# Kernel tuning notes

Measured on AMD Instinct MI355X. Metric: run time of the kernel, lower is better.

Reference implementation:

```python
import jax, jax.numpy as jnp
import numpy as np

B, T, C, H = 2, 2048, 1024, 16
D = C // H  # head dim 64

def setup_inputs() -> dict:
    key = jax.random.key(0)
    k1, k2, k3 = jax.random.split(key, 3)
    x = jax.random.normal(k1, (B, T, C), dtype=jnp.float32)
    W_attn = jax.random.normal(k2, (C, 3 * C), dtype=jnp.float32) * (1.0 / np.sqrt(C))
    b_attn = jnp.zeros((3 * C,), dtype=jnp.float32)
    W_proj = jax.random.normal(k3, (C, C), dtype=jnp.float32) * (1.0 / np.sqrt(C))
    b_proj = jnp.zeros((C,), dtype=jnp.float32)
    return {"x": x, "W_attn": W_attn, "b_attn": b_attn, "W_proj": W_proj, "b_proj": b_proj}

def reference(x, W_attn, b_attn, W_proj, b_proj):
    Bsz, Tlen, Cdim = x.shape
    qkv = x @ W_attn + b_attn  # [B,T,3C]
    q, k, v = jnp.split(qkv, 3, axis=2)
    # [B,T,C] -> [B,H,T,D]
    q = q.reshape(Bsz, Tlen, H, D).transpose(0, 2, 1, 3)
    k = k.reshape(Bsz, Tlen, H, D).transpose(0, 2, 1, 3)
    v = v.reshape(Bsz, Tlen, H, D).transpose(0, 2, 1, 3)
    att = jnp.einsum('bhqd,bhkd->bhqk', q, k) * (1.0 / np.sqrt(D))
    causal = jnp.tril(jnp.ones((Tlen, Tlen), dtype=bool))
    att = jnp.where(causal[None, None, :, :], att, jnp.float32(-jnp.inf))
    att = jax.nn.softmax(att, axis=-1)
    y = jnp.einsum('bhqk,bhkd->bhqd', att, v)  # [B,H,T,D]
    y = y.transpose(0, 2, 1, 3).reshape(Bsz, Tlen, Cdim)
    return y @ W_proj + b_proj
```

## Files before the change

### kernel.cpp

```cpp
#include <hip/hip_runtime.h>
#include <math.h>

#define BSZ 2
#define TSEQ 2048
#define CDIM 1024
#define HNUM 16

typedef __attribute__((ext_vector_type(8))) short bhalf8;
typedef __attribute__((ext_vector_type(4))) short bhalf4;
typedef __attribute__((ext_vector_type(4))) float floatx4;

__device__ __forceinline__ unsigned short f2bf(float f) {
    union { float f; unsigned u; } v;
    v.f = f;
    unsigned r = v.u + 0x7FFFu + ((v.u >> 16) & 1u);
    return (unsigned short)(r >> 16);
}

__device__ __forceinline__ floatx4 fx4_zero() { floatx4 z = {0.f,0.f,0.f,0.f}; return z; }

typedef __attribute__((address_space(3))) unsigned int lds_u32;
typedef const __attribute__((address_space(1))) unsigned int g_u32;
__device__ __forceinline__ void async_copy16(const void* g, void* l) {
    __builtin_amdgcn_global_load_lds((g_u32*)g, (lds_u32*)l, 16, 0, 0);
}

__global__ __launch_bounds__(256) void conv_bf16(
    const float* __restrict__ x, unsigned short* __restrict__ xb)
{
    size_t i = ((size_t)blockIdx.x * 256 + threadIdx.x) * 8;
    float4 a = *(const float4*)(x + i);
    float4 b = *(const float4*)(x + i + 4);
    uint4 o;
    o.x = (unsigned)f2bf(a.x) | ((unsigned)f2bf(a.y) << 16);
    o.y = (unsigned)f2bf(a.z) | ((unsigned)f2bf(a.w) << 16);
    o.z = (unsigned)f2bf(b.x) | ((unsigned)f2bf(b.y) << 16);
    o.w = (unsigned)f2bf(b.z) | ((unsigned)f2bf(b.w) << 16);
    *(uint4*)(xb + i) = o;
}

__global__ __launch_bounds__(256) void transpose_bf16(
    const float* __restrict__ W, unsigned short* __restrict__ Wt, int K, int N)
{
    __shared__ float t[32][33];
    const int n0 = blockIdx.x * 32, k0 = blockIdx.y * 32;
    const int tx = threadIdx.x & 31, ty = threadIdx.x >> 5;
#pragma unroll
    for (int i = 0; i < 4; ++i)
        t[ty + i * 8][tx] = W[(size_t)(k0 + ty + i * 8) * N + n0 + tx];
    __syncthreads();
#pragma unroll
    for (int i = 0; i < 4; ++i)
        Wt[(size_t)(n0 + ty + i * 8) * K + k0 + tx] = f2bf(t[tx][ty + i * 8]);
}

template<int BM, bool OUT_BF16>
__global__ __launch_bounds__(256) void gemm_bt(
    const unsigned short* __restrict__ A, const unsigned short* __restrict__ Bt,
    const float* __restrict__ bias, void* __restrict__ Cp,
    int M, int N, int K, int v_start, unsigned short* __restrict__ vt)
{
    constexpr int ALINES = BM / 64;
    constexpr int MT = BM / 32;
    __shared__ unsigned short As[2][BM * 32];
    __shared__ unsigned short Bs[2][128 * 32];

    const int tid   = threadIdx.x;
    const int bm    = blockIdx.y;
    const int bn    = blockIdx.x;
    const int wave  = tid >> 6;
    const int col16 = tid & 15;
    const int quad  = (tid & 63) >> 4;
    const int wm    = (wave >> 1) * (BM / 2);
    const int wn    = (wave & 1) * 64;

    floatx4 acc[MT][4];
#pragma unroll
    for (int i = 0; i < MT; ++i)
#pragma unroll
        for (int j = 0; j < 4; ++j) acc[i][j] = fx4_zero();

    const int gr = tid >> 2;
    const int gk = (tid & 3) * 8;
    const unsigned short* Ab = A  + (size_t)(bm * BM + gr) * K + gk;
    const unsigned short* Bb = Bt + (size_t)(bn * 128 + gr) * K + gk;

#define STAGE(k0, bf) { \
    char* AsB = (char*)As[bf] + wave * 1024; \
    char* BsB = (char*)Bs[bf] + wave * 1024; \
    _Pragma("unroll") \
    for (int l = 0; l < ALINES; ++l) \
        async_copy16(Ab + (size_t)l * 64 * K + (k0), AsB + l * 4096); \
    async_copy16(Bb + (k0), BsB); \
    async_copy16(Bb + (size_t)64 * K + (k0), BsB + 4096); }

#define COMPUTE(bf) { \
    bhalf8 a[MT], b[4]; \
    _Pragma("unroll") \
    for (int i = 0; i < MT; ++i) \
        a[i] = *(const bhalf8*)&As[bf][(wm + i * 16 + col16) * 32 + quad * 8]; \
    _Pragma("unroll") \
    for (int j = 0; j < 4; ++j) \
        b[j] = *(const bhalf8*)&Bs[bf][(wn + j * 16 + col16) * 32 + quad * 8]; \
    _Pragma("unroll") \
    for (int i = 0; i < MT; ++i) \
        _Pragma("unroll") \
        for (int j = 0; j < 4; ++j) \
            acc[i][j] = __builtin_amdgcn_mfma_f32_16x16x32_bf16(a[i], b[j], acc[i][j], 0, 0, 0); }

    STAGE(0, 0);
    __syncthreads();
    int buf = 0;
    for (int k0 = 0; k0 < K - 32; k0 += 32) {
        STAGE(k0 + 32, buf ^ 1);
        COMPUTE(buf);
        __syncthreads();
        buf ^= 1;
    }
    COMPUTE(buf);
#undef STAGE
#undef COMPUTE

    const int colbase = bn * 128 + wn;
    const bool vpath = (v_start >= 0) && (colbase >= v_start);
#pragma unroll
    for (int j = 0; j < 4; ++j) {
        int col = colbase + j * 16 + col16;
        float bv = bias[col];
#pragma unroll
        for (int i = 0; i < MT; ++i) {
            if (vpath) {
                int row0 = bm * BM + wm + i * 16 + quad * 4;
                ushort4 o;
                o.x = f2bf(acc[i][j][0] + bv);
                o.y = f2bf(acc[i][j][1] + bv);
                o.z = f2bf(acc[i][j][2] + bv);
                o.w = f2bf(acc[i][j][3] + bv);
                size_t vrow = (size_t)((row0 >> 11) * 1024 + (col - v_start));
                *(ushort4*)(vt + vrow * 2048 + (row0 & 2047)) = o;
            } else {
#pragma unroll
                for (int r = 0; r < 4; ++r) {
                    int row = bm * BM + wm + i * 16 + quad * 4 + r;
                    float v = acc[i][j][r] + bv;
                    if (OUT_BF16)
                        ((unsigned short*)Cp)[(size_t)row * N + col] = f2bf(v);
                    else
                        ((float*)Cp)[(size_t)row * N + col] = v;
                }
            }
        }
    }
}

template<bool DIAG>
__device__ __forceinline__ void attn_tile(
    const unsigned short* __restrict__ Ks, const unsigned short* __restrict__ Vt,
    const bhalf8* qf, floatx4* oT, float& l_part,
    int col16, int quad, int qloc)
{
    const float C_MUL = 0.125f * 1.44269504f;
    const float C_SUB = 17.31234049f;
    const int sx = col16 & 7;

    floatx4 s[4];
#pragma unroll
    for (int n = 0; n < 4; ++n) {
        const int row = 16 * n + col16;
        bhalf8 k0 = *(const bhalf8*)&Ks[row * 64 + ((quad ^ sx) * 8)];
        bhalf8 k1 = *(const bhalf8*)&Ks[row * 64 + (((4 + quad) ^ sx) * 8)];
        floatx4 t = __builtin_amdgcn_mfma_f32_16x16x32_bf16(k0, qf[0], fx4_zero(), 0, 0, 0);
        s[n] = __builtin_amdgcn_mfma_f32_16x16x32_bf16(k1, qf[1], t, 0, 0, 0);
    }

    bhalf4 pb[4];
#pragma unroll
    for (int n = 0; n < 4; ++n) {
        unsigned a[4];
#pragma unroll
        for (int r = 0; r < 4; ++r) {
            float p = exp2f(fmaf(s[n][r], C_MUL, -C_SUB));
            if (DIAG) {
                if (16 * n + quad * 4 + r > qloc) p = 0.f;
            }
            l_part += p;
            a[r] = __float_as_uint(p) + 0x8000u;
        }
        union { unsigned u[2]; bhalf4 b; } uu;
        uu.u[0] = (a[0] >> 16) | (a[1] & 0xffff0000u);
        uu.u[1] = (a[2] >> 16) | (a[3] & 0xffff0000u);
        pb[n] = uu.b;
    }

#pragma unroll
    for (int n = 0; n < 4; ++n) {
#pragma unroll
        for (int dt = 0; dt < 4; ++dt) {
            const int d = 16 * dt + col16;
            const bhalf4 av = *(const bhalf4*)&Vt[d * 76 + 16 * n + quad * 4];
            oT[dt] = __builtin_amdgcn_mfma_f32_16x16x16bf16_1k(av, pb[n], oT[dt], 0, 0, 0);
        }
    }
}

__global__ __launch_bounds__(256) void attn_mfma(
    const unsigned short* __restrict__ qkv,
    const unsigned short* __restrict__ vT,
    unsigned short* __restrict__ yout)
{
    __shared__ unsigned short Kbuf[2][64 * 64];
    __shared__ unsigned short Vbuf[2][64 * 76];

    const int tid   = threadIdx.x;
    const int wave  = tid >> 6;
    const int col16 = tid & 15;
    const int quad  = (tid & 63) >> 4;
    const int qb    = (int)gridDim.y - 1 - (int)blockIdx.y;
    const int bh    = blockIdx.x;
    const int b     = bh >> 4;
    const int h     = bh & 15;

    const unsigned short* base  = qkv + (size_t)b * TSEQ * 3072 + h * 64;
    const unsigned short* kbase = base + CDIM;
    const unsigned short* vtb   = vT + (size_t)(b * 1024 + h * 64) * 2048;

    bhalf8 qf[2];
    {
        const unsigned short* qrow =
            base + (size_t)(qb * 64 + wave * 16 + col16) * 3072 + quad * 8;
        qf[0] = *(const bhalf8*)qrow;
        qf[1] = *(const bhalf8*)(qrow + 32);
    }

    const int krow = tid >> 3;
    const int kchk = (tid & 7) ^ (krow & 7);
    const unsigned short* ksrc0 = kbase + (size_t)krow * 3072 + kchk * 8;
    const unsigned short* ksrc1 = kbase + (size_t)(krow + 32) * 3072 + kchk * 8;

    const int vd  = tid >> 3;
    const int vt0 = (tid & 7) * 8;
    const unsigned short* vsrc0 = vtb + (size_t)vd * 2048 + vt0;
    const unsigned short* vsrc1 = vtb + (size_t)(vd + 32) * 2048 + vt0;

#define KSTAGE(kb, bf) { \
    char* Kd = (char*)Kbuf[bf] + wave * 1024; \
    async_copy16(ksrc0 + (size_t)(kb) * 64 * 3072, Kd); \
    async_copy16(ksrc1 + (size_t)(kb) * 64 * 3072, Kd + 4096); }

    floatx4 oT[4];
#pragma unroll
    for (int dt = 0; dt < 4; ++dt) oT[dt] = fx4_zero();
    float l_part = 0.f;
    const int qloc = wave * 16 + col16;

    {
        uint4 nv0 = *(const uint4*)vsrc0;
        uint4 nv1 = *(const uint4*)vsrc1;
        KSTAGE(0, 0);
        *(uint4*)&Vbuf[0][vd * 76 + vt0]        = nv0;
        *(uint4*)&Vbuf[0][(vd + 32) * 76 + vt0] = nv1;
    }
    __syncthreads();
    int buf = 0;
    for (int kb = 0; kb < qb; ++kb) {
        uint4 nv0 = *(const uint4*)(vsrc0 + (size_t)(kb + 1) * 64);
        uint4 nv1 = *(const uint4*)(vsrc1 + (size_t)(kb + 1) * 64);
        KSTAGE(kb + 1, buf ^ 1);
        attn_tile<false>(Kbuf[buf], Vbuf[buf], qf, oT, l_part, col16, quad, qloc);
        *(uint4*)&Vbuf[buf ^ 1][vd * 76 + vt0]        = nv0;
        *(uint4*)&Vbuf[buf ^ 1][(vd + 32) * 76 + vt0] = nv1;
        __syncthreads();
        buf ^= 1;
    }
    attn_tile<true>(Kbuf[buf], Vbuf[buf], qf, oT, l_part, col16, quad, qloc);
#undef KSTAGE

    float l = l_part;
    l += __shfl_xor(l, 16);
    l += __shfl_xor(l, 32);
    const float inv = 1.0f / l;
    const size_t row = (size_t)b * TSEQ + (size_t)qb * 64 + wave * 16 + col16;
#pragma unroll
    for (int dt = 0; dt < 4; ++dt) {
        ushort4 o;
        o.x = f2bf(oT[dt][0] * inv);
        o.y = f2bf(oT[dt][1] * inv);
        o.z = f2bf(oT[dt][2] * inv);
        o.w = f2bf(oT[dt][3] * inv);
        *(ushort4*)(yout + row * CDIM + h * 64 + 16 * dt + quad * 4) = o;
    }
}

extern "C" void kernel_launch(void* const* d_in, const int* in_sizes, int n_in,
                              void* d_out, int out_size, void* d_ws, size_t ws_size,
                              hipStream_t stream)
{
    const float* x      = (const float*)d_in[0];
    const float* W_attn = (const float*)d_in[1];
    const float* b_attn = (const float*)d_in[2];
    const float* W_proj = (const float*)d_in[3];
    const float* b_proj = (const float*)d_in[4];
    float* out = (float*)d_out;

    unsigned short* qkv = (unsigned short*)d_ws;
    unsigned short* y   = qkv + (size_t)4096 * 3072;
    unsigned short* xb  = y   + (size_t)4096 * 1024;
    unsigned short* WtA = xb  + (size_t)4096 * 1024;
    unsigned short* WtP = WtA + (size_t)3072 * 1024;
    unsigned short* vT  = WtP + (size_t)1024 * 1024;

    conv_bf16<<<dim3((4096 * 1024) / (256 * 8)), 256, 0, stream>>>(x, xb);
    transpose_bf16<<<dim3(3072 / 32, 1024 / 32), 256, 0, stream>>>(W_attn, WtA, 1024, 3072);
    transpose_bf16<<<dim3(1024 / 32, 1024 / 32), 256, 0, stream>>>(W_proj, WtP, 1024, 1024);

    gemm_bt<128, true><<<dim3(3072 / 128, 4096 / 128), 256, 0, stream>>>(
        xb, WtA, b_attn, qkv, 4096, 3072, 1024, 2048, vT);
    attn_mfma<<<dim3(BSZ * HNUM, TSEQ / 64), 256, 0, stream>>>(qkv, vT, y);
    gemm_bt<64, false><<<dim3(1024 / 128, 4096 / 64), 256, 0, stream>>>(
        y, WtP, b_proj, out, 4096, 1024, 1024, -1, nullptr);
}
```

Before: 188.4 us.

## Fuse prepass kernels, split-K projection, and widen attention blocks to 128 queries

Merges the input conversion and two weight transposes into one prepass launch. Splits the output projection GEMM over two K halves that accumulate into a zeroed output with atomic adds. Moves attention to 512-thread blocks covering 128 query rows, where each K/V tile is loaded once per block and shared by more waves, and the softmax exponent prep uses packed float2 math. The changes target launch overhead, reuse of K/V loads, and projection parallelism, at the cost of an extra memset, atomic traffic on the output, and fewer attention blocks with more threads each.

```diff
diff --git a/kernel.cpp b/kernel.cpp
--- a/kernel.cpp
+++ b/kernel.cpp
@@ -9,6 +9,7 @@
 typedef __attribute__((ext_vector_type(8))) short bhalf8;
 typedef __attribute__((ext_vector_type(4))) short bhalf4;
 typedef __attribute__((ext_vector_type(4))) float floatx4;
+typedef __attribute__((ext_vector_type(2))) float floatx2;
 
 __device__ __forceinline__ unsigned short f2bf(float f) {
     union { float f; unsigned u; } v;
@@ -25,26 +26,11 @@
     __builtin_amdgcn_global_load_lds((g_u32*)g, (lds_u32*)l, 16, 0, 0);
 }
 
-__global__ __launch_bounds__(256) void conv_bf16(
-    const float* __restrict__ x, unsigned short* __restrict__ xb)
-{
-    size_t i = ((size_t)blockIdx.x * 256 + threadIdx.x) * 8;
-    float4 a = *(const float4*)(x + i);
-    float4 b = *(const float4*)(x + i + 4);
-    uint4 o;
-    o.x = (unsigned)f2bf(a.x) | ((unsigned)f2bf(a.y) << 16);
-    o.y = (unsigned)f2bf(a.z) | ((unsigned)f2bf(a.w) << 16);
-    o.z = (unsigned)f2bf(b.x) | ((unsigned)f2bf(b.y) << 16);
-    o.w = (unsigned)f2bf(b.z) | ((unsigned)f2bf(b.w) << 16);
-    *(uint4*)(xb + i) = o;
-}
-
-__global__ __launch_bounds__(256) void transpose_bf16(
-    const float* __restrict__ W, unsigned short* __restrict__ Wt, int K, int N)
-{
-    __shared__ float t[32][33];
-    const int n0 = blockIdx.x * 32, k0 = blockIdx.y * 32;
-    const int tx = threadIdx.x & 31, ty = threadIdx.x >> 5;
+__device__ __forceinline__ void trans_tile(
+    const float* __restrict__ W, unsigned short* __restrict__ Wt,
+    int K, int N, int n0, int k0, int tid, float (*t)[33])
+{
+    const int tx = tid & 31, ty = tid >> 5;
 #pragma unroll
     for (int i = 0; i < 4; ++i)
         t[ty + i * 8][tx] = W[(size_t)(k0 + ty + i * 8) * N + n0 + tx];
@@ -54,15 +40,39 @@
         Wt[(size_t)(n0 + ty + i * 8) * K + k0 + tx] = f2bf(t[tx][ty + i * 8]);
 }
 
-template<int BM, bool OUT_BF16>
-__global__ __launch_bounds__(256) void gemm_bt(
+__global__ __launch_bounds__(256) void prepass(
+    const float* __restrict__ x, unsigned short* __restrict__ xb,
+    const float* __restrict__ Wa, unsigned short* __restrict__ WtA,
+    const float* __restrict__ Wp, unsigned short* __restrict__ WtP)
+{
+    __shared__ float t[32][33];
+    const int bid = blockIdx.x;
+    const int tid = threadIdx.x;
+    if (bid < 2048) {
+        size_t i = ((size_t)bid * 256 + tid) * 8;
+        float4 a = *(const float4*)(x + i);
+        float4 b = *(const float4*)(x + i + 4);
+        uint4 o;
+        o.x = (unsigned)f2bf(a.x) | ((unsigned)f2bf(a.y) << 16);
+        o.y = (unsigned)f2bf(a.z) | ((unsigned)f2bf(a.w) << 16);
+        o.z = (unsigned)f2bf(b.x) | ((unsigned)f2bf(b.y) << 16);
+        o.w = (unsigned)f2bf(b.z) | ((unsigned)f2bf(b.w) << 16);
+        *(uint4*)(xb + i) = o;
+    } else if (bid < 5120) {
+        int tl = bid - 2048;
+        trans_tile(Wa, WtA, 1024, 3072, (tl % 96) * 32, (tl / 96) * 32, tid, t);
+    } else {
+        int tl = bid - 5120;
+        trans_tile(Wp, WtP, 1024, 1024, (tl % 32) * 32, (tl / 32) * 32, tid, t);
+    }
+}
+
+__global__ __launch_bounds__(256) void gemm_qkv(
     const unsigned short* __restrict__ A, const unsigned short* __restrict__ Bt,
-    const float* __restrict__ bias, void* __restrict__ Cp,
+    const float* __restrict__ bias, unsigned short* __restrict__ Cp,
     int M, int N, int K, int v_start, unsigned short* __restrict__ vt)
 {
-    constexpr int ALINES = BM / 64;
-    constexpr int MT = BM / 32;
-    __shared__ unsigned short As[2][BM * 32];
+    __shared__ unsigned short As[2][128 * 32];
     __shared__ unsigned short Bs[2][128 * 32];
 
     const int tid   = threadIdx.x;
@@ -71,66 +81,65 @@
     const int wave  = tid >> 6;
     const int col16 = tid & 15;
     const int quad  = (tid & 63) >> 4;
-    const int wm    = (wave >> 1) * (BM / 2);
+    const int wm    = (wave >> 1) * 64;
     const int wn    = (wave & 1) * 64;
 
-    floatx4 acc[MT][4];
-#pragma unroll
-    for (int i = 0; i < MT; ++i)
+    floatx4 acc[4][4];
+#pragma unroll
+    for (int i = 0; i < 4; ++i)
 #pragma unroll
         for (int j = 0; j < 4; ++j) acc[i][j] = fx4_zero();
 
     const int gr = tid >> 2;
     const int gk = (tid & 3) * 8;
-    const unsigned short* Ab = A  + (size_t)(bm * BM + gr) * K + gk;
+    const unsigned short* Ab = A  + (size_t)(bm * 128 + gr) * K + gk;
     const unsigned short* Bb = Bt + (size_t)(bn * 128 + gr) * K + gk;
 
-#define STAGE(k0, bf) { \
+#define QSTAGE(k0, bf) { \
     char* AsB = (char*)As[bf] + wave * 1024; \
     char* BsB = (char*)Bs[bf] + wave * 1024; \
-    _Pragma("unroll") \
-    for (int l = 0; l < ALINES; ++l) \
-        async_copy16(Ab + (size_t)l * 64 * K + (k0), AsB + l * 4096); \
-    async_copy16(Bb + (k0), BsB); \
+    async_copy16(Ab + (k0),                  AsB); \
+    async_copy16(Ab + (size_t)64 * K + (k0), AsB + 4096); \
+    async_copy16(Bb + (k0),                  BsB); \
     async_copy16(Bb + (size_t)64 * K + (k0), BsB + 4096); }
 
-#define COMPUTE(bf) { \
-    bhalf8 a[MT], b[4]; \
-    _Pragma("unroll") \
-    for (int i = 0; i < MT; ++i) \
+#define QCOMPUTE(bf) { \
+    bhalf8 a[4], b[4]; \
+    _Pragma("unroll") \
+    for (int i = 0; i < 4; ++i) \
         a[i] = *(const bhalf8*)&As[bf][(wm + i * 16 + col16) * 32 + quad * 8]; \
     _Pragma("unroll") \
     for (int j = 0; j < 4; ++j) \
         b[j] = *(const bhalf8*)&Bs[bf][(wn + j * 16 + col16) * 32 + quad * 8]; \
     _Pragma("unroll") \
-    for (int i = 0; i < MT; ++i) \
+    for (int i = 0; i < 4; ++i) \
         _Pragma("unroll") \
         for (int j = 0; j < 4; ++j) \
             acc[i][j] = __builtin_amdgcn_mfma_f32_16x16x32_bf16(a[i], b[j], acc[i][j], 0, 0, 0); }
 
-    STAGE(0, 0);
+    QSTAGE(0, 0);
     __syncthreads();
     int buf = 0;
     for (int k0 = 0; k0 < K - 32; k0 += 32) {
-        STAGE(k0 + 32, buf ^ 1);
-        COMPUTE(buf);
+        QSTAGE(k0 + 32, buf ^ 1);
+        QCOMPUTE(buf);
         __syncthreads();
         buf ^= 1;
     }
-    COMPUTE(buf);
-#undef STAGE
-#undef COMPUTE
+    QCOMPUTE(buf);
+#undef QSTAGE
+#undef QCOMPUTE
 
     const int colbase = bn * 128 + wn;
-    const bool vpath = (v_start >= 0) && (colbase >= v_start);
+    const bool vpath = colbase >= v_start;
 #pragma unroll
     for (int j = 0; j < 4; ++j) {
         int col = colbase + j * 16 + col16;
         float bv = bias[col];
 #pragma unroll
-        for (int i = 0; i < MT; ++i) {
+        for (int i = 0; i < 4; ++i) {
             if (vpath) {
-                int row0 = bm * BM + wm + i * 16 + quad * 4;
+                int row0 = bm * 128 + wm + i * 16 + quad * 4;
                 ushort4 o;
                 o.x = f2bf(acc[i][j][0] + bv);
                 o.y = f2bf(acc[i][j][1] + bv);
@@ -141,22 +150,97 @@
             } else {
 #pragma unroll
                 for (int r = 0; r < 4; ++r) {
-                    int row = bm * BM + wm + i * 16 + quad * 4 + r;
-                    float v = acc[i][j][r] + bv;
-                    if (OUT_BF16)
-                        ((unsigned short*)Cp)[(size_t)row * N + col] = f2bf(v);
-                    else
-                        ((float*)Cp)[(size_t)row * N + col] = v;
+                    int row = bm * 128 + wm + i * 16 + quad * 4 + r;
+                    Cp[(size_t)row * N + col] = f2bf(acc[i][j][r] + bv);
                 }
             }
         }
     }
 }
 
-template<bool DIAG>
+__global__ __launch_bounds__(256) void gemm_proj_sk(
+    const unsigned short* __restrict__ A, const unsigned short* __restrict__ Bt,
+    const float* __restrict__ bias, float* __restrict__ out,
+    int M, int N, int K)
+{
+    __shared__ unsigned short As[2][64 * 32];
+    __shared__ unsigned short Bs[2][128 * 32];
+
+    const int tid   = threadIdx.x;
+    const int bm    = blockIdx.y;
+    const int bn    = blockIdx.x;
+    const int koff  = blockIdx.z * (K / 2);
+    const int wave  = tid >> 6;
+    const int col16 = tid & 15;
+    const int quad  = (tid & 63) >> 4;
+    const int wm    = (wave >> 1) * 32;
+    const int wn    = (wave & 1) * 64;
+
+    floatx4 acc[2][4];
+#pragma unroll
+    for (int i = 0; i < 2; ++i)
+#pragma unroll
+        for (int j = 0; j < 4; ++j) acc[i][j] = fx4_zero();
+
+    const int gr = tid >> 2;
+    const int gk = (tid & 3) * 8;
+    const unsigned short* Ab = A  + (size_t)(bm * 64 + gr) * K + koff + gk;
+    const unsigned short* Bb = Bt + (size_t)(bn * 128 + gr) * K + koff + gk;
+
+#define PSTAGE(k0, bf) { \
+    char* AsB = (char*)As[bf] + wave * 1024; \
+    char* BsB = (char*)Bs[bf] + wave * 1024; \
+    async_copy16(Ab + (k0),                  AsB); \
+    async_copy16(Bb + (k0),                  BsB); \
+    async_copy16(Bb + (size_t)64 * K + (k0), BsB + 4096); }
+
+#define PCOMPUTE(bf) { \
+    bhalf8 a[2], b[4]; \
+    _Pragma("unroll") \
+    for (int i = 0; i < 2; ++i) \
+        a[i] = *(const bhalf8*)&As[bf][(wm + i * 16 + col16) * 32 + quad * 8]; \
+    _Pragma("unroll") \
+    for (int j = 0; j < 4; ++j) \
+        b[j] = *(const bhalf8*)&Bs[bf][(wn + j * 16 + col16) * 32 + quad * 8]; \
+    _Pragma("unroll") \
+    for (int i = 0; i < 2; ++i) \
+        _Pragma("unroll") \
+        for (int j = 0; j < 4; ++j) \
+            acc[i][j] = __builtin_amdgcn_mfma_f32_16x16x32_bf16(a[i], b[j], acc[i][j], 0, 0, 0); }
+
+    PSTAGE(0, 0);
+    __syncthreads();
+    int buf = 0;
+    for (int k0 = 0; k0 < K / 2 - 32; k0 += 32) {
+        PSTAGE(k0 + 32, buf ^ 1);
+        PCOMPUTE(buf);
+        __syncthreads();
+        buf ^= 1;
+    }
+    PCOMPUTE(buf);
+#undef PSTAGE
+#undef PCOMPUTE
+
+    const bool addb = (koff == 0);
+#pragma unroll
+    for (int j = 0; j < 4; ++j) {
+        int col = bn * 128 + wn + j * 16 + col16;
+        float bv = addb ? bias[col] : 0.f;
+#pragma unroll
+        for (int i = 0; i < 2; ++i) {
+#pragma unroll
+            for (int r = 0; r < 4; ++r) {
+                int row = bm * 64 + wm + i * 16 + quad * 4 + r;
+                unsafeAtomicAdd(&out[(size_t)row * N + col], acc[i][j][r] + bv);
+            }
+        }
+    }
+}
+
+template<int DIAGOFF>
 __device__ __forceinline__ void attn_tile(
     const unsigned short* __restrict__ Ks, const unsigned short* __restrict__ Vt,
-    const bhalf8* qf, floatx4* oT, float& l_part,
+    const bhalf8* qf, floatx4* oT, floatx2& l2,
     int col16, int quad, int qloc)
 {
     const float C_MUL = 0.125f * 1.44269504f;
@@ -176,19 +260,28 @@
     bhalf4 pb[4];
 #pragma unroll
     for (int n = 0; n < 4; ++n) {
-        unsigned a[4];
-#pragma unroll
-        for (int r = 0; r < 4; ++r) {
-            float p = exp2f(fmaf(s[n][r], C_MUL, -C_SUB));
-            if (DIAG) {
-                if (16 * n + quad * 4 + r > qloc) p = 0.f;
-            }
-            l_part += p;
-            a[r] = __float_as_uint(p) + 0x8000u;
+        floatx2 a01 = {s[n][0], s[n][1]};
+        floatx2 a23 = {s[n][2], s[n][3]};
+        a01 = a01 * C_MUL - C_SUB;
+        a23 = a23 * C_MUL - C_SUB;
+        float p[4];
+        p[0] = exp2f(a01[0]); p[1] = exp2f(a01[1]);
+        p[2] = exp2f(a23[0]); p[3] = exp2f(a23[1]);
+        if (DIAGOFF >= 0) {
+#pragma unroll
+            for (int r = 0; r < 4; ++r)
+                if (16 * n + quad * 4 + r + DIAGOFF > qloc) p[r] = 0.f;
         }
+        floatx2 p01 = {p[0], p[1]}, p23 = {p[2], p[3]};
+        l2 += p01;
+        l2 += p23;
+        unsigned a0 = __float_as_uint(p[0]) + 0x8000u;
+        unsigned a1 = __float_as_uint(p[1]) + 0x8000u;
+        unsigned a2 = __float_as_uint(p[2]) + 0x8000u;
+        unsigned a3 = __float_as_uint(p[3]) + 0x8000u;
         union { unsigned u[2]; bhalf4 b; } uu;
-        uu.u[0] = (a[0] >> 16) | (a[1] & 0xffff0000u);
-        uu.u[1] = (a[2] >> 16) | (a[3] & 0xffff0000u);
+        uu.u[0] = (a0 >> 16) | (a1 & 0xffff0000u);
+        uu.u[1] = (a2 >> 16) | (a3 & 0xffff0000u);
         pb[n] = uu.b;
     }
 
@@ -203,7 +296,7 @@
     }
 }
 
-__global__ __launch_bounds__(256) void attn_mfma(
+__global__ __launch_bounds__(512) void attn_mfma(
     const unsigned short* __restrict__ qkv,
     const unsigned short* __restrict__ vT,
     unsigned short* __restrict__ yout)
@@ -227,59 +320,59 @@
     bhalf8 qf[2];
     {
         const unsigned short* qrow =
-            base + (size_t)(qb * 64 + wave * 16 + col16) * 3072 + quad * 8;
+            base + (size_t)(qb * 128 + wave * 16 + col16) * 3072 + quad * 8;
         qf[0] = *(const bhalf8*)qrow;
         qf[1] = *(const bhalf8*)(qrow + 32);
     }
 
     const int krow = tid >> 3;
     const int kchk = (tid & 7) ^ (krow & 7);
-    const unsigned short* ksrc0 = kbase + (size_t)krow * 3072 + kchk * 8;
-    const unsigned short* ksrc1 = kbase + (size_t)(krow + 32) * 3072 + kchk * 8;
-
+    const unsigned short* ksrc = kbase + (size_t)krow * 3072 + kchk * 8;
     const int vd  = tid >> 3;
     const int vt0 = (tid & 7) * 8;
-    const unsigned short* vsrc0 = vtb + (size_t)vd * 2048 + vt0;
-    const unsigned short* vsrc1 = vtb + (size_t)(vd + 32) * 2048 + vt0;
-
-#define KSTAGE(kb, bf) { \
-    char* Kd = (char*)Kbuf[bf] + wave * 1024; \
-    async_copy16(ksrc0 + (size_t)(kb) * 64 * 3072, Kd); \
-    async_copy16(ksrc1 + (size_t)(kb) * 64 * 3072, Kd + 4096); }
+    const unsigned short* vsrc = vtb + (size_t)vd * 2048 + vt0;
+
+#define KSTAGE(kb, bf) \
+    async_copy16(ksrc + (size_t)(kb) * 64 * 3072, (char*)Kbuf[bf] + wave * 1024);
 
     floatx4 oT[4];
 #pragma unroll
     for (int dt = 0; dt < 4; ++dt) oT[dt] = fx4_zero();
-    float l_part = 0.f;
+    floatx2 l2 = {0.f, 0.f};
     const int qloc = wave * 16 + col16;
 
     {
-        uint4 nv0 = *(const uint4*)vsrc0;
-        uint4 nv1 = *(const uint4*)vsrc1;
+        uint4 nv = *(const uint4*)vsrc;
         KSTAGE(0, 0);
-        *(uint4*)&Vbuf[0][vd * 76 + vt0]        = nv0;
-        *(uint4*)&Vbuf[0][(vd + 32) * 76 + vt0] = nv1;
+        *(uint4*)&Vbuf[0][vd * 76 + vt0] = nv;
     }
     __syncthreads();
     int buf = 0;
-    for (int kb = 0; kb < qb; ++kb) {
-        uint4 nv0 = *(const uint4*)(vsrc0 + (size_t)(kb + 1) * 64);
-        uint4 nv1 = *(const uint4*)(vsrc1 + (size_t)(kb + 1) * 64);
+    const int nfull = 2 * qb;
+    for (int kb = 0; kb < nfull; ++kb) {
+        uint4 nv = *(const uint4*)(vsrc + (size_t)(kb + 1) * 64);
         KSTAGE(kb + 1, buf ^ 1);
-        attn_tile<false>(Kbuf[buf], Vbuf[buf], qf, oT, l_part, col16, quad, qloc);
-        *(uint4*)&Vbuf[buf ^ 1][vd * 76 + vt0]        = nv0;
-        *(uint4*)&Vbuf[buf ^ 1][(vd + 32) * 76 + vt0] = nv1;
+        attn_tile<-1>(Kbuf[buf], Vbuf[buf], qf, oT, l2, col16, quad, qloc);
+        *(uint4*)&Vbuf[buf ^ 1][vd * 76 + vt0] = nv;
         __syncthreads();
         buf ^= 1;
     }
-    attn_tile<true>(Kbuf[buf], Vbuf[buf], qf, oT, l_part, col16, quad, qloc);
+    {
+        uint4 nv = *(const uint4*)(vsrc + (size_t)(nfull + 1) * 64);
+        KSTAGE(nfull + 1, buf ^ 1);
+        attn_tile<0>(Kbuf[buf], Vbuf[buf], qf, oT, l2, col16, quad, qloc);
+        *(uint4*)&Vbuf[buf ^ 1][vd * 76 + vt0] = nv;
+        __syncthreads();
+        buf ^= 1;
+        attn_tile<64>(Kbuf[buf], Vbuf[buf], qf, oT, l2, col16, quad, qloc);
+    }
 #undef KSTAGE
 
-    float l = l_part;
+    float l = l2[0] + l2[1];
     l += __shfl_xor(l, 16);
     l += __shfl_xor(l, 32);
     const float inv = 1.0f / l;
-    const size_t row = (size_t)b * TSEQ + (size_t)qb * 64 + wave * 16 + col16;
+    const size_t row = (size_t)b * TSEQ + (size_t)qb * 128 + wave * 16 + col16;
 #pragma unroll
     for (int dt = 0; dt < 4; ++dt) {
         ushort4 o;
@@ -309,13 +402,14 @@
     unsigned short* WtP = WtA + (size_t)3072 * 1024;
     unsigned short* vT  = WtP + (size_t)1024 * 1024;
 
-    conv_bf16<<<dim3((4096 * 1024) / (256 * 8)), 256, 0, stream>>>(x, xb);
-    transpose_bf16<<<dim3(3072 / 32, 1024 / 32), 256, 0, stream>>>(W_attn, WtA, 1024, 3072);
-    transpose_bf16<<<dim3(1024 / 32, 1024 / 32), 256, 0, stream>>>(W_proj, WtP, 1024, 1024);
-
-    gemm_bt<128, true><<<dim3(3072 / 128, 4096 / 128), 256, 0, stream>>>(
+    prepass<<<dim3(6144), 256, 0, stream>>>(x, xb, W_attn, WtA, W_proj, WtP);
+
+    gemm_qkv<<<dim3(3072 / 128, 4096 / 128), 256, 0, stream>>>(
         xb, WtA, b_attn, qkv, 4096, 3072, 1024, 2048, vT);
-    attn_mfma<<<dim3(BSZ * HNUM, TSEQ / 64), 256, 0, stream>>>(qkv, vT, y);
-    gemm_bt<64, false><<<dim3(1024 / 128, 4096 / 64), 256, 0, stream>>>(
-        y, WtP, b_proj, out, 4096, 1024, 1024, -1, nullptr);
-}
+
+    attn_mfma<<<dim3(BSZ * HNUM, TSEQ / 128), 512, 0, stream>>>(qkv, vT, y);
+
+    hipMemsetAsync(out, 0, (size_t)4096 * 1024 * sizeof(float), stream);
+    gemm_proj_sk<<<dim3(1024 / 128, 4096 / 64, 2), 256, 0, stream>>>(
+        y, WtP, b_proj, out, 4096, 1024, 1024);
+}
```

Result: slower. 215.8 us (+14.5%).
